# Performance work log

Measured on AMD Instinct MI355X. Metric: run time of the kernel, lower is better.

Reference implementation:

```python
import jax, jax.numpy as jnp
from jax import lax
import numpy as np
import math


def make_kernel():
    # StyleGAN2 blur kernel [1,3,3,1], normalized outer product
    k = jnp.array([1.0, 3.0, 3.0, 1.0], dtype=jnp.float32)
    k2 = jnp.outer(k, k)
    return k2 / jnp.sum(k2)


def upfirdn2d(x, kernel, up=1, pad=(0, 0)):
    # x: [B,C,H,W]; depthwise FIR filter, optional zero-insert upsampling
    C = x.shape[1]
    w = jnp.tile(jnp.flip(kernel)[None, None].astype(x.dtype), (C, 1, 1, 1))
    # torch upfirdn pads up-1 trailing zeros after the last sample; lhs_dilation
    # only inserts zeros between samples, so fold the extra zeros into pad[1].
    p = (pad[0], pad[1] + up - 1)
    return lax.conv_general_dilated(
        x, w, (1, 1), (p, p), lhs_dilation=(up, up), feature_group_count=C)


def modulated_conv(x, weight, style, demodulate=True, up=False):
    # per-sample weight modulation + demodulation, executed as grouped conv
    B, Cin, H, W = x.shape
    Cout, _, k, _ = weight.shape
    scale = 1.0 / math.sqrt(Cin * k * k)
    w = scale * weight[None] * style[:, None, :, None, None]  # [B,Cout,Cin,k,k]
    if demodulate:
        d = lax.rsqrt(jnp.sum(w * w, axis=(2, 3, 4)) + 1e-8)
        w = w * d[:, :, None, None, None]
    xg = x.reshape(1, B * Cin, H, W)
    if up:
        # conv_transpose2d(stride=2, pad=0) == lhs-dilated conv with flipped kernel
        wg = jnp.flip(w, (-2, -1)).reshape(B * Cout, Cin, k, k)
        out = lax.conv_general_dilated(
            xg, wg, (1, 1), ((k - 1, k - 1), (k - 1, k - 1)),
            lhs_dilation=(2, 2), feature_group_count=B)
    else:
        pad = k // 2
        out = lax.conv_general_dilated(
            xg, w.reshape(B * Cout, Cin, k, k), (1, 1),
            ((pad, pad), (pad, pad)), feature_group_count=B)
    return out.reshape(B, Cout, out.shape[2], out.shape[3])


def fused_lrelu(x, bias):
    y = x + bias[None, :, None, None]
    return jnp.where(y >= 0, y, 0.2 * y) * math.sqrt(2.0)


def setup_inputs() -> dict:
    key = jax.random.key(0)
    ks = jax.random.split(key, 12)
    B, C, H = 8, 512, 32
    f = jnp.float32
    return {
        "x": jax.random.normal(ks[0], (B, C, H, H), f),
        "skip": jax.random.normal(ks[1], (B, 3, H, H), f),
        "w1": jax.random.normal(ks[2], (C, C, 3, 3), f),
        "b1": jnp.zeros((C,), f),
        "s1": jax.random.normal(ks[3], (B, C), f),
        "nw1": jax.random.normal(ks[4], (1,), f) * 0.1,
        "n1": jax.random.normal(ks[5], (B, 1, 2 * H, 2 * H), f),
        "w2": jax.random.normal(ks[6], (C, C, 3, 3), f),
        "b2": jnp.zeros((C,), f),
        "s2": jax.random.normal(ks[7], (B, C), f),
        "nw2": jax.random.normal(ks[8], (1,), f) * 0.1,
        "n2": jax.random.normal(ks[9], (B, 1, 2 * H, 2 * H), f),
        "w_rgb": jax.random.normal(ks[10], (3, C, 1, 1), f),
        "b_rgb": jnp.zeros((3,), f),
        "s_rgb": jax.random.normal(ks[11], (B, C), f),
    }


def reference(x, skip, w1, b1, s1, nw1, n1, w2, b2, s2, nw2, n2,
              w_rgb, b_rgb, s_rgb):
    kern = make_kernel()
    # conv1: upsampling modulated conv + blur (Blur with upsample_factor=2)
    out = modulated_conv(x, w1, s1, demodulate=True, up=True)
    out = upfirdn2d(out, kern * 4.0, up=1, pad=(1, 1))
    out = out + nw1 * n1          # NoiseInjection
    out = fused_lrelu(out, b1)    # FusedLeakyReLU
    # conv2: plain modulated conv
    out = modulated_conv(out, w2, s2, demodulate=True)
    out = out + nw2 * n2
    out = fused_lrelu(out, b2)
    # ToRGB: 1x1 mod conv, no demodulation, + bias; skip = rgb + upsample(skip)
    rgb = modulated_conv(out, w_rgb, s_rgb, demodulate=False)
    rgb = rgb + b_rgb[None, :, None, None]
    skip_up = upfirdn2d(skip, kern * 4.0, up=2, pad=(2, 1))
    return rgb + skip_up
```

## Files before the change

### kernel.cpp

```cpp
#include <hip/hip_runtime.h>
#include <stdint.h>

typedef unsigned short ushort_t;
typedef unsigned int uint_t;
typedef __bf16 bf16x8 __attribute__((ext_vector_type(8)));
typedef float f32x4 __attribute__((ext_vector_type(4)));

#define GLOBAL_AS __attribute__((address_space(1)))
#define LDS_AS    __attribute__((address_space(3)))

#define SCALE_CONV 0.014731391f
#define SCALE_RGB  0.044194174f
#define SQRT2_F    1.41421356237f

__device__ __forceinline__ void async_cp16(const void* g, void* l) {
  __builtin_amdgcn_global_load_lds((const GLOBAL_AS uint_t*)g,
                                   (LDS_AS uint_t*)l, 16, 0, 0);
}
__device__ __forceinline__ ushort_t f2bf(float v) {
  union { float f; uint_t u; } c; c.f = v;
  uint_t r = c.u + 0x7fffu + ((c.u >> 16) & 1u);
  return (ushort_t)(r >> 16);
}
__device__ __forceinline__ float bf2f(ushort_t u) {
  union { uint_t u; float f; } c; c.u = ((uint_t)u) << 16;
  return c.f;
}

__global__ __launch_bounds__(256) void prep_x1(
    const float* __restrict__ x, const float* __restrict__ s1,
    ushort_t* __restrict__ xpad) {
  __shared__ ushort_t t[32 * 520];
  const int b  = blockIdx.x >> 5;
  const int j1 = blockIdx.x & 31;
  for (int idx = threadIdx.x; idx < 512 * 32; idx += 256) {
    int ci = idx >> 5, j2 = idx & 31;
    float v = x[(size_t)(b * 512 + ci) * 1024 + j1 * 32 + j2];
    v *= s1[b * 512 + ci] * SCALE_CONV;
    t[j2 * 520 + ci] = f2bf(v);
  }
  __syncthreads();
  for (int idx = threadIdx.x; idx < 32 * 512; idx += 256) {
    int j2 = idx >> 9, ci = idx & 511;
    xpad[((size_t)(b * 34 + j1 + 1) * 34 + (j2 + 1)) * 512 + ci] = t[j2 * 520 + ci];
  }
}

__global__ __launch_bounds__(256) void prep_w(
    const float* __restrict__ w1, const float* __restrict__ w2,
    ushort_t* __restrict__ wt1, ushort_t* __restrict__ wt2,
    float* __restrict__ wsqT1, float* __restrict__ wsqT2) {
  int t = blockIdx.x * 256 + threadIdx.x;
  const float* w  = (t < 262144) ? w1 : w2;
  ushort_t*   wt  = (t < 262144) ? wt1 : wt2;
  float*      wq  = (t < 262144) ? wsqT1 : wsqT2;
  int tt = t & 262143;
  int ci = tt & 511, co = tt >> 9;
  const float* wp = w + (size_t)(co * 512 + ci) * 9;
  float sq = 0.f;
#pragma unroll
  for (int u = 0; u < 9; ++u) {
    float v = wp[u];
    sq += v * v;
    wt[((size_t)u * 512 + co) * 512 + ci] = f2bf(v);
  }
  wq[ci * 512 + co] = sq;
}

__global__ __launch_bounds__(512) void demod2(
    const float* __restrict__ wsqT1, const float* __restrict__ s1, float* __restrict__ d1,
    const float* __restrict__ wsqT2, const float* __restrict__ s2, float* __restrict__ d2) {
  const float* wq = blockIdx.y ? wsqT2 : wsqT1;
  const float* s  = blockIdx.y ? s2 : s1;
  float*       d  = blockIdx.y ? d2 : d1;
  const int b  = blockIdx.x;
  const int co = threadIdx.x;
  __shared__ float ssq[512];
  float sv = s[b * 512 + co];
  ssq[co] = sv * sv;
  __syncthreads();
  float a = 0.f;
#pragma unroll 4
  for (int ci = 0; ci < 512; ++ci) a += wq[ci * 512 + co] * ssq[ci];
  d[b * 512 + co] = rsqrtf(a * (1.f / 4608.f) + 1e-8f);
}

__global__ __launch_bounds__(256) void border_zero(
    ushort_t* __restrict__ xpad, ushort_t* __restrict__ ypad, ushort_t* __restrict__ opad) {
  const int z = blockIdx.z;
  ushort_t* p = (z == 0) ? xpad : (z == 1 ? ypad : opad);
  const int W = (z == 0) ? 34 : (z == 1 ? 67 : 66);
  const int nb = 4 * W - 4;
  const int t = blockIdx.x * 256 + threadIdx.x;
  const int pix = t >> 6, ch = (t & 63) * 8;
  if (pix >= nb) return;
  const int b = blockIdx.y;
  int y, x;
  if (pix < W)          { y = 0;     x = pix; }
  else if (pix < 2 * W) { y = W - 1; x = pix - W; }
  else { int q = pix - 2 * W; y = 1 + (q >> 1); x = (q & 1) ? W - 1 : 0; }
  uint4 z4 = {0, 0, 0, 0};
  *(uint4*)(p + ((size_t)(b * W + y) * W + x) * 512 + ch) = z4;
}

__constant__ int           c_ph_off[4]  = {0, 4, 6, 8};
__constant__ int           c_ph_ntap[4] = {4, 2, 2, 1};
__constant__ unsigned char c_tap_u1[9]  = {0,0,1,1, 0,1, 1,1, 1};
__constant__ unsigned char c_tap_u2[9]  = {0,1,0,1, 1,1, 0,1, 1};
__constant__ unsigned char c_tap_pl[9]  = {8,6,2,0, 7,1, 5,3, 4};

template <int MODE>
__global__ __launch_bounds__(256, 3) void gemm_conv(
    const ushort_t* __restrict__ inp, const ushort_t* __restrict__ wt,
    const float* __restrict__ dmod, const float* __restrict__ noise,
    const float* __restrict__ nw, const float* __restrict__ bias,
    const float* __restrict__ snext, float snext_scale,
    ushort_t* __restrict__ outp) {
  __shared__ ushort_t ldsA[128 * 64];
  __shared__ ushort_t ldsB[128 * 64];

  const int tid  = threadIdx.x;
  const int lane = tid & 63;
  const int wv   = tid >> 6;
  const int wm   = wv & 1;
  const int wn   = wv >> 1;
  const int l16  = lane & 15;
  const int quad = lane >> 4;

  const int mtile = blockIdx.x;
  const int ntile = blockIdx.y;
  const int a  = (MODE == 0) ? blockIdx.z : 0;
  const int a1 = a >> 1, a2 = a & 1;

  const int cl = ((lane & 7) - (lane >> 3)) & 7;
  const char* pA[4];
  const char* pB[4];
#pragma unroll
  for (int t = 0; t < 4; ++t) {
    int row = wv * 32 + t * 8 + (lane >> 3);
    int m   = mtile * 128 + row;
    size_t pix;
    if (MODE == 0) {
      if (m > 8711) m = 8711;
      int b = m / 1089, rr = m % 1089;
      int p1 = rr / 33, p2 = rr % 33;
      pix = ((size_t)(b * 34 + p1) * 34 + p2) * 512;
    } else {
      int b = m >> 12, o1 = (m >> 6) & 63, o2 = m & 63;
      pix = ((size_t)(b * 66 + o1 + 1) * 66 + (o2 + 1)) * 512;
    }
    pA[t] = (const char*)inp + pix * 2 + cl * 16;
    int n = ntile * 128 + row;
    pB[t] = (const char*)wt + (size_t)n * 1024 + cl * 16;
  }
  char* dstA[4];
  char* dstB[4];
#pragma unroll
  for (int t = 0; t < 4; ++t) {
    dstA[t] = (char*)ldsA + wv * 4096 + t * 1024;
    dstB[t] = (char*)ldsB + wv * 4096 + t * 1024;
  }

  int offA[4], offB[4];
#pragma unroll
  for (int i = 0; i < 4; ++i) {
    int r  = wm * 64 + i * 16 + l16;
    int rn = wn * 64 + i * 16 + l16;
    offA[i] = r  * 64 + (((quad + r)  & 7) << 3);
    offB[i] = rn * 64 + (((quad + rn) & 7) << 3);
  }

  f32x4 acc[4][4];
#pragma unroll
  for (int i = 0; i < 4; ++i)
#pragma unroll
    for (int j = 0; j < 4; ++j) acc[i][j] = (f32x4){0.f, 0.f, 0.f, 0.f};

  const int ntap = (MODE == 0) ? c_ph_ntap[a] : 9;
#pragma unroll 1
  for (int ti = 0; ti < ntap; ++ti) {
    int aoff, boff;
    if (MODE == 0) {
      int e = c_ph_off[a] + ti;
      aoff = ((int)c_tap_u1[e] * 34 + (int)c_tap_u2[e]) * 1024;
      boff = (int)c_tap_pl[e] * 524288;
    } else {
      aoff = ((ti / 3 - 1) * 66 + (ti % 3 - 1)) * 1024;
      boff = ti * 524288;
    }
#pragma unroll 1
    for (int kc = 0; kc < 8; ++kc) {
      const int koff = kc * 128;
      __syncthreads();
#pragma unroll
      for (int t = 0; t < 4; ++t) async_cp16(pA[t] + aoff + koff, dstA[t]);
#pragma unroll
      for (int t = 0; t < 4; ++t) async_cp16(pB[t] + boff + koff, dstB[t]);
      __syncthreads();
#pragma unroll
      for (int kk = 0; kk < 2; ++kk) {
        const int kx = kk << 5;
        bf16x8 af[4], bg[4];
#pragma unroll
        for (int i = 0; i < 4; ++i) af[i] = *reinterpret_cast<const bf16x8*>(ldsA + (offA[i] ^ kx));
#pragma unroll
        for (int j = 0; j < 4; ++j) bg[j] = *reinterpret_cast<const bf16x8*>(ldsB + (offB[j] ^ kx));
#pragma unroll
        for (int i = 0; i < 4; ++i)
#pragma unroll
          for (int j = 0; j < 4; ++j)
            acc[i][j] = __builtin_amdgcn_mfma_f32_16x16x32_bf16(af[i], bg[j], acc[i][j], 0, 0, 0);
      }
    }
  }

  int co_[4];
#pragma unroll
  for (int j = 0; j < 4; ++j) co_[j] = ntile * 128 + wn * 64 + j * 16 + l16;

  if (MODE == 0) {
#pragma unroll
    for (int i = 0; i < 4; ++i) {
#pragma unroll
      for (int r = 0; r < 4; ++r) {
        int m = mtile * 128 + wm * 64 + i * 16 + quad * 4 + r;
        if (m < 8712) {
          int b = m / 1089, rr = m % 1089;
          int p1 = rr / 33, p2 = rr % 33;
          if ((a1 == 0 || p1 < 32) && (a2 == 0 || p2 < 32)) {
            int o1 = 2 * p1 + a1, o2 = 2 * p2 + a2;
            size_t ob = ((size_t)(b * 67 + o1 + 1) * 67 + (o2 + 1)) * 512;
#pragma unroll
            for (int j = 0; j < 4; ++j)
              outp[ob + co_[j]] = f2bf(acc[i][j][r] * dmod[b * 512 + co_[j]]);
          }
        }
      }
    }
  } else {
    const int b = mtile >> 5;
    const float nwv = nw[0];
    float dj_[4], sj_[4], bj_[4];
#pragma unroll
    for (int j = 0; j < 4; ++j) {
      dj_[j] = dmod[b * 512 + co_[j]];
      sj_[j] = snext[b * 512 + co_[j]] * snext_scale;
      bj_[j] = bias[co_[j]];
    }
#pragma unroll
    for (int i = 0; i < 4; ++i) {
#pragma unroll
      for (int r = 0; r < 4; ++r) {
        int m = mtile * 128 + wm * 64 + i * 16 + quad * 4 + r;
        int o1 = (m >> 6) & 63, o2 = m & 63;
        float nz = nwv * noise[(b << 12) + (o1 << 6) + o2];
        size_t ob = ((size_t)(b * 64 + o1) * 64 + o2) * 512;
#pragma unroll
        for (int j = 0; j < 4; ++j) {
          float v = acc[i][j][r] * dj_[j] + nz + bj_[j];
          v = (v >= 0.f ? v : 0.2f * v) * SQRT2_F;
          v *= sj_[j];
          outp[ob + co_[j]] = f2bf(v);
        }
      }
    }
  }
}

__global__ __launch_bounds__(256) void blur_noise_act(
    const ushort_t* __restrict__ y1pad, const float* __restrict__ noise,
    const float* __restrict__ nw, const float* __restrict__ bias,
    const float* __restrict__ s2, ushort_t* __restrict__ out1pad) {
  const int cg  = threadIdx.x & 63;
  const int pg  = blockIdx.x * 4 + (threadIdx.x >> 6);
  const int b   = pg >> 10;
  const int q1  = (pg >> 4) & 63;
  const int q2g = (pg & 15) * 4;
  const float cw[4] = {0.25f, 0.75f, 0.75f, 0.25f};

  float acc[4][8];
#pragma unroll
  for (int j = 0; j < 4; ++j)
#pragma unroll
    for (int e = 0; e < 8; ++e) acc[j][e] = 0.f;

#pragma unroll
  for (int t2 = 0; t2 < 7; ++t2) {
    int cc = q2g + t2;
    float vt[8];
#pragma unroll
    for (int e = 0; e < 8; ++e) vt[e] = 0.f;
#pragma unroll
    for (int t1 = 0; t1 < 4; ++t1) {
      const ushort_t* p = y1pad + ((size_t)(b * 67 + q1 + t1) * 67 + cc) * 512 + cg * 8;
      ushort_t v[8];
      *(uint4*)v = *(const uint4*)p;
#pragma unroll
      for (int e = 0; e < 8; ++e) vt[e] += cw[t1] * bf2f(v[e]);
    }
#pragma unroll
    for (int j = 0; j < 4; ++j) {
      int t = t2 - j;
      if (t >= 0 && t < 4) {
#pragma unroll
        for (int e = 0; e < 8; ++e) acc[j][e] += cw[t] * vt[e];
      }
    }
  }

  const float nwv = nw[0];
  float bj[8], sj[8];
#pragma unroll
  for (int e = 0; e < 8; ++e) {
    bj[e] = bias[cg * 8 + e];
    sj[e] = s2[b * 512 + cg * 8 + e] * SCALE_CONV;
  }
#pragma unroll
  for (int j = 0; j < 4; ++j) {
    int q2 = q2g + j;
    float nz = nwv * noise[(b << 12) + (q1 << 6) + q2];
    ushort_t o[8];
#pragma unroll
    for (int e = 0; e < 8; ++e) {
      float v = acc[j][e] + nz + bj[e];
      v = (v >= 0.f ? v : 0.2f * v) * SQRT2_F * sj[e];
      o[e] = f2bf(v);
    }
    *(uint4*)(out1pad + ((size_t)(b * 66 + q1 + 1) * 66 + (q2 + 1)) * 512 + cg * 8) = *(uint4*)o;
  }
}

__global__ __launch_bounds__(256) void torgb_skip(
    const ushort_t* __restrict__ out2s, const float* __restrict__ wrgb,
    const float* __restrict__ brgb, const float* __restrict__ skip,
    float* __restrict__ out) {
  const int lane = threadIdx.x & 63;
  const int pix  = blockIdx.x * 4 + (threadIdx.x >> 6);
  const int b = pix >> 12, o1 = (pix >> 6) & 63, o2 = pix & 63;
  const ushort_t* src = out2s + (size_t)pix * 512 + lane * 8;
  ushort_t v[8];
  *(uint4*)v = *(const uint4*)src;
  float s0 = 0.f, s1 = 0.f, s2 = 0.f;
#pragma unroll
  for (int e = 0; e < 8; ++e) {
    float xv = bf2f(v[e]);
    int ci = lane * 8 + e;
    s0 += xv * wrgb[ci];
    s1 += xv * wrgb[512 + ci];
    s2 += xv * wrgb[1024 + ci];
  }
#pragma unroll
  for (int o = 32; o; o >>= 1) {
    s0 += __shfl_xor(s0, o);
    s1 += __shfl_xor(s1, o);
    s2 += __shfl_xor(s2, o);
  }
  if (lane < 3) {
    float v3 = (lane == 0) ? s0 : (lane == 1 ? s1 : s2);
    int P1 = o1 >> 1, P2 = o2 >> 1;
    int jy0, jy1, jx0, jx1;
    float wy0, wy1, wx0, wx1;
    if ((o1 & 1) == 0) { jy0 = P1 - 1; wy0 = .25f; jy1 = P1;     wy1 = .75f; }
    else               { jy0 = P1;     wy0 = .75f; jy1 = P1 + 1; wy1 = .25f; }
    if ((o2 & 1) == 0) { jx0 = P2 - 1; wx0 = .25f; jx1 = P2;     wx1 = .75f; }
    else               { jx0 = P2;     wx0 = .75f; jx1 = P2 + 1; wx1 = .25f; }
    const float* sp = skip + (size_t)(b * 3 + lane) * 1024;
    float sv = 0.f;
    if (jy0 >= 0 && jy0 < 32) {
      if (jx0 >= 0 && jx0 < 32) sv += wy0 * wx0 * sp[jy0 * 32 + jx0];
      if (jx1 >= 0 && jx1 < 32) sv += wy0 * wx1 * sp[jy0 * 32 + jx1];
    }
    if (jy1 >= 0 && jy1 < 32) {
      if (jx0 >= 0 && jx0 < 32) sv += wy1 * wx0 * sp[jy1 * 32 + jx0];
      if (jx1 >= 0 && jx1 < 32) sv += wy1 * wx1 * sp[jy1 * 32 + jx1];
    }
    out[((size_t)(b * 3 + lane) << 12) + (o1 << 6) + o2] = v3 + brgb[lane] + sv;
  }
}

extern "C" void kernel_launch(void* const* d_in, const int* in_sizes, int n_in,
                              void* d_out, int out_size, void* d_ws, size_t ws_size,
                              hipStream_t stream) {
  const float* x    = (const float*)d_in[0];
  const float* skip = (const float*)d_in[1];
  const float* w1   = (const float*)d_in[2];
  const float* b1   = (const float*)d_in[3];
  const float* s1   = (const float*)d_in[4];
  const float* nw1  = (const float*)d_in[5];
  const float* n1   = (const float*)d_in[6];
  const float* w2   = (const float*)d_in[7];
  const float* b2   = (const float*)d_in[8];
  const float* s2   = (const float*)d_in[9];
  const float* nw2  = (const float*)d_in[10];
  const float* n2   = (const float*)d_in[11];
  const float* wrgb = (const float*)d_in[12];
  const float* brgb = (const float*)d_in[13];
  const float* srgb = (const float*)d_in[14];

  char* ws = (char*)d_ws;
  const size_t XPAD_B  = (size_t)8 * 34 * 34 * 512 * 2;
  const size_t Y1PAD_B = (size_t)8 * 67 * 67 * 512 * 2;
  const size_t OUT1_B  = (size_t)8 * 66 * 66 * 512 * 2;
  const size_t WT_B    = (size_t)9 * 512 * 512 * 2;
  size_t off = 0;
  ushort_t* xpad1   = (ushort_t*)(ws + off); off += XPAD_B;
  ushort_t* y1pad   = (ushort_t*)(ws + off); off += Y1PAD_B;
  ushort_t* out1pad = (ushort_t*)(ws + off); off += OUT1_B;
  ushort_t* wt1     = (ushort_t*)(ws + off); off += WT_B;
  ushort_t* wt2     = (ushort_t*)(ws + off); off += WT_B;
  float*    d1      = (float*)(ws + off);    off += 8 * 512 * 4;
  float*    d2      = (float*)(ws + off);    off += 8 * 512 * 4;
  ushort_t* out2s  = y1pad;
  float*    wsqT1  = (float*)y1pad;
  float*    wsqT2  = wsqT1 + 512 * 512;

  prep_x1<<<256, 256, 0, stream>>>(x, s1, xpad1);
  prep_w<<<2048, 256, 0, stream>>>(w1, w2, wt1, wt2, wsqT1, wsqT2);
  demod2<<<dim3(8, 2), 512, 0, stream>>>(wsqT1, s1, d1, wsqT2, s2, d2);
  border_zero<<<dim3(66, 8, 3), 256, 0, stream>>>(xpad1, y1pad, out1pad);

  gemm_conv<0><<<dim3(69, 4, 4), 256, 0, stream>>>(
      xpad1, wt1, d1, nullptr, nullptr, nullptr, nullptr, 0.f, y1pad);
  blur_noise_act<<<2048, 256, 0, stream>>>(y1pad, n1, nw1, b1, s2, out1pad);
  gemm_conv<1><<<dim3(256, 4, 1), 256, 0, stream>>>(
      out1pad, wt2, d2, n2, nw2, b2, srgb, SCALE_RGB, out2s);
  torgb_skip<<<8192, 256, 0, stream>>>(out2s, wrgb, brgb, skip, (float*)d_out);
}
```

Before: 393.8 us.

## Double-buffer LDS in conv2 GEMM to overlap async loads with MFMA

Splits the templated GEMM into two kernels and gives the second 3x3 conv a double-buffered LDS pipeline over a flattened 72-step tap×K loop. The next stage's global-to-LDS async copies are issued before computing on the current buffer, with partial vmcnt waits, so load latency can overlap the MFMA work. LDS use doubles and occupancy is lowered to 2 blocks per CU. Hand-written s_barrier and waitcnt asm adds risk if the compiler reorders or counts loads differently.

```diff
diff --git a/kernel.cpp b/kernel.cpp
--- a/kernel.cpp
+++ b/kernel.cpp
@@ -109,13 +109,9 @@
 __constant__ unsigned char c_tap_u2[9]  = {0,1,0,1, 1,1, 0,1, 1};
 __constant__ unsigned char c_tap_pl[9]  = {8,6,2,0, 7,1, 5,3, 4};
 
-template <int MODE>
-__global__ __launch_bounds__(256, 3) void gemm_conv(
+__global__ __launch_bounds__(256, 3) void gemm_conv1(
     const ushort_t* __restrict__ inp, const ushort_t* __restrict__ wt,
-    const float* __restrict__ dmod, const float* __restrict__ noise,
-    const float* __restrict__ nw, const float* __restrict__ bias,
-    const float* __restrict__ snext, float snext_scale,
-    ushort_t* __restrict__ outp) {
+    const float* __restrict__ dmod, ushort_t* __restrict__ outp) {
   __shared__ ushort_t ldsA[128 * 64];
   __shared__ ushort_t ldsB[128 * 64];
 
@@ -129,7 +125,7 @@
 
   const int mtile = blockIdx.x;
   const int ntile = blockIdx.y;
-  const int a  = (MODE == 0) ? blockIdx.z : 0;
+  const int a  = blockIdx.z;
   const int a1 = a >> 1, a2 = a & 1;
 
   const int cl = ((lane & 7) - (lane >> 3)) & 7;
@@ -139,16 +135,10 @@
   for (int t = 0; t < 4; ++t) {
     int row = wv * 32 + t * 8 + (lane >> 3);
     int m   = mtile * 128 + row;
-    size_t pix;
-    if (MODE == 0) {
-      if (m > 8711) m = 8711;
-      int b = m / 1089, rr = m % 1089;
-      int p1 = rr / 33, p2 = rr % 33;
-      pix = ((size_t)(b * 34 + p1) * 34 + p2) * 512;
-    } else {
-      int b = m >> 12, o1 = (m >> 6) & 63, o2 = m & 63;
-      pix = ((size_t)(b * 66 + o1 + 1) * 66 + (o2 + 1)) * 512;
-    }
+    if (m > 8711) m = 8711;
+    int b = m / 1089, rr = m % 1089;
+    int p1 = rr / 33, p2 = rr % 33;
+    size_t pix = ((size_t)(b * 34 + p1) * 34 + p2) * 512;
     pA[t] = (const char*)inp + pix * 2 + cl * 16;
     int n = ntile * 128 + row;
     pB[t] = (const char*)wt + (size_t)n * 1024 + cl * 16;
@@ -176,18 +166,12 @@
 #pragma unroll
     for (int j = 0; j < 4; ++j) acc[i][j] = (f32x4){0.f, 0.f, 0.f, 0.f};
 
-  const int ntap = (MODE == 0) ? c_ph_ntap[a] : 9;
+  const int ntap = c_ph_ntap[a];
 #pragma unroll 1
   for (int ti = 0; ti < ntap; ++ti) {
-    int aoff, boff;
-    if (MODE == 0) {
-      int e = c_ph_off[a] + ti;
-      aoff = ((int)c_tap_u1[e] * 34 + (int)c_tap_u2[e]) * 1024;
-      boff = (int)c_tap_pl[e] * 524288;
-    } else {
-      aoff = ((ti / 3 - 1) * 66 + (ti % 3 - 1)) * 1024;
-      boff = ti * 524288;
-    }
+    int e = c_ph_off[a] + ti;
+    int aoff = ((int)c_tap_u1[e] * 34 + (int)c_tap_u2[e]) * 1024;
+    int boff = (int)c_tap_pl[e] * 524288;
 #pragma unroll 1
     for (int kc = 0; kc < 8; ++kc) {
       const int koff = kc * 128;
@@ -218,50 +202,144 @@
 #pragma unroll
   for (int j = 0; j < 4; ++j) co_[j] = ntile * 128 + wn * 64 + j * 16 + l16;
 
-  if (MODE == 0) {
-#pragma unroll
-    for (int i = 0; i < 4; ++i) {
-#pragma unroll
-      for (int r = 0; r < 4; ++r) {
-        int m = mtile * 128 + wm * 64 + i * 16 + quad * 4 + r;
-        if (m < 8712) {
-          int b = m / 1089, rr = m % 1089;
-          int p1 = rr / 33, p2 = rr % 33;
-          if ((a1 == 0 || p1 < 32) && (a2 == 0 || p2 < 32)) {
-            int o1 = 2 * p1 + a1, o2 = 2 * p2 + a2;
-            size_t ob = ((size_t)(b * 67 + o1 + 1) * 67 + (o2 + 1)) * 512;
-#pragma unroll
-            for (int j = 0; j < 4; ++j)
-              outp[ob + co_[j]] = f2bf(acc[i][j][r] * dmod[b * 512 + co_[j]]);
-          }
+#pragma unroll
+  for (int i = 0; i < 4; ++i) {
+#pragma unroll
+    for (int r = 0; r < 4; ++r) {
+      int m = mtile * 128 + wm * 64 + i * 16 + quad * 4 + r;
+      if (m < 8712) {
+        int b = m / 1089, rr = m % 1089;
+        int p1 = rr / 33, p2 = rr % 33;
+        if ((a1 == 0 || p1 < 32) && (a2 == 0 || p2 < 32)) {
+          int o1 = 2 * p1 + a1, o2 = 2 * p2 + a2;
+          size_t ob = ((size_t)(b * 67 + o1 + 1) * 67 + (o2 + 1)) * 512;
+#pragma unroll
+          for (int j = 0; j < 4; ++j)
+            outp[ob + co_[j]] = f2bf(acc[i][j][r] * dmod[b * 512 + co_[j]]);
         }
       }
     }
-  } else {
-    const int b = mtile >> 5;
-    const float nwv = nw[0];
-    float dj_[4], sj_[4], bj_[4];
-#pragma unroll
-    for (int j = 0; j < 4; ++j) {
-      dj_[j] = dmod[b * 512 + co_[j]];
-      sj_[j] = snext[b * 512 + co_[j]] * snext_scale;
-      bj_[j] = bias[co_[j]];
-    }
-#pragma unroll
-    for (int i = 0; i < 4; ++i) {
-#pragma unroll
-      for (int r = 0; r < 4; ++r) {
-        int m = mtile * 128 + wm * 64 + i * 16 + quad * 4 + r;
-        int o1 = (m >> 6) & 63, o2 = m & 63;
-        float nz = nwv * noise[(b << 12) + (o1 << 6) + o2];
-        size_t ob = ((size_t)(b * 64 + o1) * 64 + o2) * 512;
-#pragma unroll
-        for (int j = 0; j < 4; ++j) {
-          float v = acc[i][j][r] * dj_[j] + nz + bj_[j];
-          v = (v >= 0.f ? v : 0.2f * v) * SQRT2_F;
-          v *= sj_[j];
-          outp[ob + co_[j]] = f2bf(v);
-        }
+  }
+}
+
+__global__ __launch_bounds__(256, 2) void gemm_conv2_pipe(
+    const ushort_t* __restrict__ inp, const ushort_t* __restrict__ wt,
+    const float* __restrict__ dmod, const float* __restrict__ noise,
+    const float* __restrict__ nw, const float* __restrict__ bias,
+    const float* __restrict__ snext, float snext_scale,
+    ushort_t* __restrict__ outp) {
+  __shared__ ushort_t ldsA[2 * 128 * 64];
+  __shared__ ushort_t ldsB[2 * 128 * 64];
+
+  const int tid  = threadIdx.x;
+  const int lane = tid & 63;
+  const int wv   = tid >> 6;
+  const int wm   = wv & 1;
+  const int wn   = wv >> 1;
+  const int l16  = lane & 15;
+  const int quad = lane >> 4;
+
+  const int mtile = blockIdx.x;
+  const int ntile = blockIdx.y;
+
+  const int cl = ((lane & 7) - (lane >> 3)) & 7;
+  const char* pA[4];
+  const char* pB[4];
+#pragma unroll
+  for (int t = 0; t < 4; ++t) {
+    int row = wv * 32 + t * 8 + (lane >> 3);
+    int m   = mtile * 128 + row;
+    int b = m >> 12, o1 = (m >> 6) & 63, o2 = m & 63;
+    size_t pix = ((size_t)(b * 66 + o1 + 1) * 66 + (o2 + 1)) * 512;
+    pA[t] = (const char*)inp + pix * 2 + cl * 16;
+    int n = ntile * 128 + row;
+    pB[t] = (const char*)wt + (size_t)n * 1024 + cl * 16;
+  }
+
+  int offA[4], offB[4];
+#pragma unroll
+  for (int i = 0; i < 4; ++i) {
+    int r  = wm * 64 + i * 16 + l16;
+    int rn = wn * 64 + i * 16 + l16;
+    offA[i] = r  * 64 + (((quad + r)  & 7) << 3);
+    offB[i] = rn * 64 + (((quad + rn) & 7) << 3);
+  }
+
+  f32x4 acc[4][4];
+#pragma unroll
+  for (int i = 0; i < 4; ++i)
+#pragma unroll
+    for (int j = 0; j < 4; ++j) acc[i][j] = (f32x4){0.f, 0.f, 0.f, 0.f};
+
+  auto stagef = [&](int k, int sel) {
+    int tap = k >> 3, kc = k & 7;
+    int ty = tap * 86 >> 8;
+    int tx = tap - ty * 3;
+    int aoff = ((ty - 1) * 66 + (tx - 1)) * 1024 + kc * 128;
+    int boff = tap * 524288 + kc * 128;
+    char* dA = (char*)ldsA + sel * 16384 + wv * 4096;
+    char* dB = (char*)ldsB + sel * 16384 + wv * 4096;
+#pragma unroll
+    for (int t = 0; t < 4; ++t) async_cp16(pA[t] + aoff, dA + t * 1024);
+#pragma unroll
+    for (int t = 0; t < 4; ++t) async_cp16(pB[t] + boff, dB + t * 1024);
+  };
+
+  stagef(0, 0);
+#pragma unroll 1
+  for (int k = 0; k < 72; ++k) {
+    asm volatile("s_barrier" ::: "memory");
+    if (k < 71) {
+      stagef(k + 1, (k + 1) & 1);
+      asm volatile("s_waitcnt vmcnt(8)" ::: "memory");
+    } else {
+      asm volatile("s_waitcnt vmcnt(0)" ::: "memory");
+    }
+    asm volatile("s_barrier" ::: "memory");
+    const ushort_t* bA = ldsA + (k & 1) * 8192;
+    const ushort_t* bB = ldsB + (k & 1) * 8192;
+#pragma unroll
+    for (int kk = 0; kk < 2; ++kk) {
+      const int kx = kk << 5;
+      bf16x8 af[4], bg[4];
+#pragma unroll
+      for (int i = 0; i < 4; ++i) af[i] = *reinterpret_cast<const bf16x8*>(bA + (offA[i] ^ kx));
+#pragma unroll
+      for (int j = 0; j < 4; ++j) bg[j] = *reinterpret_cast<const bf16x8*>(bB + (offB[j] ^ kx));
+#pragma unroll
+      for (int i = 0; i < 4; ++i)
+#pragma unroll
+        for (int j = 0; j < 4; ++j)
+          acc[i][j] = __builtin_amdgcn_mfma_f32_16x16x32_bf16(af[i], bg[j], acc[i][j], 0, 0, 0);
+    }
+  }
+
+  const int b = mtile >> 5;
+  int co_[4];
+#pragma unroll
+  for (int j = 0; j < 4; ++j) co_[j] = ntile * 128 + wn * 64 + j * 16 + l16;
+  const float nwv = nw[0];
+  float dj_[4], sj_[4], bj_[4];
+#pragma unroll
+  for (int j = 0; j < 4; ++j) {
+    dj_[j] = dmod[b * 512 + co_[j]];
+    sj_[j] = snext[b * 512 + co_[j]] * snext_scale;
+    bj_[j] = bias[co_[j]];
+  }
+#pragma unroll
+  for (int i = 0; i < 4; ++i) {
+#pragma unroll
+    for (int r = 0; r < 4; ++r) {
+      int m = mtile * 128 + wm * 64 + i * 16 + quad * 4 + r;
+      int o1 = (m >> 6) & 63, o2 = m & 63;
+      float nz = nwv * noise[(b << 12) + (o1 << 6) + o2];
+      size_t ob = ((size_t)(b * 64 + o1) * 64 + o2) * 512;
+#pragma unroll
+      for (int j = 0; j < 4; ++j) {
+        float v = acc[i][j][r] * dj_[j] + nz + bj_[j];
+        v = (v >= 0.f ? v : 0.2f * v) * SQRT2_F;
+        v *= sj_[j];
+        outp[ob + co_[j]] = f2bf(v);
       }
     }
   }
@@ -419,10 +497,9 @@
   demod2<<<dim3(8, 2), 512, 0, stream>>>(wsqT1, s1, d1, wsqT2, s2, d2);
   border_zero<<<dim3(66, 8, 3), 256, 0, stream>>>(xpad1, y1pad, out1pad);
 
-  gemm_conv<0><<<dim3(69, 4, 4), 256, 0, stream>>>(
-      xpad1, wt1, d1, nullptr, nullptr, nullptr, nullptr, 0.f, y1pad);
+  gemm_conv1<<<dim3(69, 4, 4), 256, 0, stream>>>(xpad1, wt1, d1, y1pad);
   blur_noise_act<<<2048, 256, 0, stream>>>(y1pad, n1, nw1, b1, s2, out1pad);
-  gemm_conv<1><<<dim3(256, 4, 1), 256, 0, stream>>>(
+  gemm_conv2_pipe<<<dim3(256, 4), 256, 0, stream>>>(
       out1pad, wt2, d2, n2, nw2, b2, srgb, SCALE_RGB, out2s);
   torgb_skip<<<8192, 256, 0, stream>>>(out2s, wrgb, brgb, skip, (float*)d_out);
 }
```

Measured after the change: 407.0 us. 3.4% more time.

## Double-buffer GEMM K loop, fuse ToRGB into conv2 epilogue, split demod

Applied to the files above, without the earlier changes.

Restructures the implicit-GEMM conv kernel to use a 32-wide K step with double-buffered LDS. The next chunk is prefetched asynchronously while the current one feeds the MFMAs, and occupancy is raised to 4 blocks. The conv2 epilogue now does the 1x1 ToRGB projection directly, reducing across lanes and atomically adding into a small fp32 buffer. This removes the bf16 write and re-read of the full 512-channel activation. A light finish kernel adds bias and the upsampled skip, and the demod kernel is split across more blocks; float atomics make the summation order nondeterministic.

```diff
diff --git a/kernel.cpp b/kernel.cpp
--- a/kernel.cpp
+++ b/kernel.cpp
@@ -67,27 +67,47 @@
   wq[ci * 512 + co] = sq;
 }
 
-__global__ __launch_bounds__(512) void demod2(
+__global__ __launch_bounds__(256) void demod3(
     const float* __restrict__ wsqT1, const float* __restrict__ s1, float* __restrict__ d1,
     const float* __restrict__ wsqT2, const float* __restrict__ s2, float* __restrict__ d2) {
-  const float* wq = blockIdx.y ? wsqT2 : wsqT1;
-  const float* s  = blockIdx.y ? s2 : s1;
-  float*       d  = blockIdx.y ? d2 : d1;
-  const int b  = blockIdx.x;
-  const int co = threadIdx.x;
+  const float* wq = blockIdx.z ? wsqT2 : wsqT1;
+  const float* s  = blockIdx.z ? s2 : s1;
+  float*       d  = blockIdx.z ? d2 : d1;
+  const int b   = blockIdx.y;
+  const int co  = blockIdx.x * 64 + (threadIdx.x & 63);
+  const int cig = threadIdx.x >> 6;
   __shared__ float ssq[512];
-  float sv = s[b * 512 + co];
-  ssq[co] = sv * sv;
+  __shared__ float red[4][64];
+  for (int i = threadIdx.x; i < 512; i += 256) {
+    float v = s[b * 512 + i];
+    ssq[i] = v * v;
+  }
   __syncthreads();
   float a = 0.f;
 #pragma unroll 4
-  for (int ci = 0; ci < 512; ++ci) a += wq[ci * 512 + co] * ssq[ci];
-  d[b * 512 + co] = rsqrtf(a * (1.f / 4608.f) + 1e-8f);
+  for (int ci = cig * 128; ci < cig * 128 + 128; ++ci)
+    a += wq[ci * 512 + co] * ssq[ci];
+  red[cig][threadIdx.x & 63] = a;
+  __syncthreads();
+  if (cig == 0) {
+    int l = threadIdx.x & 63;
+    float tot = red[0][l] + red[1][l] + red[2][l] + red[3][l];
+    d[b * 512 + co] = rsqrtf(tot * (1.f / 4608.f) + 1e-8f);
+  }
 }
 
 __global__ __launch_bounds__(256) void border_zero(
-    ushort_t* __restrict__ xpad, ushort_t* __restrict__ ypad, ushort_t* __restrict__ opad) {
+    ushort_t* __restrict__ xpad, ushort_t* __restrict__ ypad, ushort_t* __restrict__ opad,
+    float* __restrict__ rgbpart) {
   const int z = blockIdx.z;
+  if (z == 3) {
+    int i = (blockIdx.y * 66 + blockIdx.x) * 256 + threadIdx.x;
+    if (i < 24576) {
+      uint4 z4 = {0, 0, 0, 0};
+      *(uint4*)(rgbpart + i * 4) = z4;
+    }
+    return;
+  }
   ushort_t* p = (z == 0) ? xpad : (z == 1 ? ypad : opad);
   const int W = (z == 0) ? 34 : (z == 1 ? 67 : 66);
   const int nb = 4 * W - 4;
@@ -110,14 +130,14 @@
 __constant__ unsigned char c_tap_pl[9]  = {8,6,2,0, 7,1, 5,3, 4};
 
 template <int MODE>
-__global__ __launch_bounds__(256, 3) void gemm_conv(
+__global__ __launch_bounds__(256, 4) void gemm_conv_p(
     const ushort_t* __restrict__ inp, const ushort_t* __restrict__ wt,
     const float* __restrict__ dmod, const float* __restrict__ noise,
     const float* __restrict__ nw, const float* __restrict__ bias,
-    const float* __restrict__ snext, float snext_scale,
-    ushort_t* __restrict__ outp) {
-  __shared__ ushort_t ldsA[128 * 64];
-  __shared__ ushort_t ldsB[128 * 64];
+    const float* __restrict__ srgb, const float* __restrict__ wrgb,
+    float* __restrict__ rgbpart, ushort_t* __restrict__ outp) {
+  __shared__ ushort_t ldsA[2 * 4096];
+  __shared__ ushort_t ldsB[2 * 4096];
 
   const int tid  = threadIdx.x;
   const int lane = tid & 63;
@@ -131,13 +151,15 @@
   const int ntile = blockIdx.y;
   const int a  = (MODE == 0) ? blockIdx.z : 0;
   const int a1 = a >> 1, a2 = a & 1;
-
-  const int cl = ((lane & 7) - (lane >> 3)) & 7;
-  const char* pA[4];
-  const char* pB[4];
-#pragma unroll
-  for (int t = 0; t < 4; ++t) {
-    int row = wv * 32 + t * 8 + (lane >> 3);
+  const int phoff = (MODE == 0) ? c_ph_off[a] : 0;
+  const int nk    = (MODE == 0) ? c_ph_ntap[a] * 16 : 144;
+
+  const int cl = ((lane & 3) - (lane >> 3)) & 3;
+  const char* pA[2];
+  const char* pB[2];
+#pragma unroll
+  for (int t = 0; t < 2; ++t) {
+    int row = wv * 32 + t * 16 + (lane >> 2);
     int m   = mtile * 128 + row;
     size_t pix;
     if (MODE == 0) {
@@ -153,21 +175,14 @@
     int n = ntile * 128 + row;
     pB[t] = (const char*)wt + (size_t)n * 1024 + cl * 16;
   }
-  char* dstA[4];
-  char* dstB[4];
-#pragma unroll
-  for (int t = 0; t < 4; ++t) {
-    dstA[t] = (char*)ldsA + wv * 4096 + t * 1024;
-    dstB[t] = (char*)ldsB + wv * 4096 + t * 1024;
-  }
 
   int offA[4], offB[4];
 #pragma unroll
   for (int i = 0; i < 4; ++i) {
     int r  = wm * 64 + i * 16 + l16;
     int rn = wn * 64 + i * 16 + l16;
-    offA[i] = r  * 64 + (((quad + r)  & 7) << 3);
-    offB[i] = rn * 64 + (((quad + rn) & 7) << 3);
+    offA[i] = r  * 32 + (((quad + (r  >> 1)) & 3) << 3);
+    offB[i] = rn * 32 + (((quad + (rn >> 1)) & 3) << 3);
   }
 
   f32x4 acc[4][4];
@@ -176,42 +191,50 @@
 #pragma unroll
     for (int j = 0; j < 4; ++j) acc[i][j] = (f32x4){0.f, 0.f, 0.f, 0.f};
 
-  const int ntap = (MODE == 0) ? c_ph_ntap[a] : 9;
-#pragma unroll 1
-  for (int ti = 0; ti < ntap; ++ti) {
+  auto stagef = [&](int kn, int sel) {
+    int tap = kn >> 4, kc = kn & 15;
     int aoff, boff;
     if (MODE == 0) {
-      int e = c_ph_off[a] + ti;
-      aoff = ((int)c_tap_u1[e] * 34 + (int)c_tap_u2[e]) * 1024;
-      boff = (int)c_tap_pl[e] * 524288;
+      int e = phoff + tap;
+      aoff = ((int)c_tap_u1[e] * 34 + (int)c_tap_u2[e]) * 1024 + kc * 64;
+      boff = (int)c_tap_pl[e] * 524288 + kc * 64;
     } else {
-      aoff = ((ti / 3 - 1) * 66 + (ti % 3 - 1)) * 1024;
-      boff = ti * 524288;
-    }
+      int ty = (tap * 86) >> 8;
+      int tx = tap - ty * 3;
+      aoff = ((ty - 1) * 66 + (tx - 1)) * 1024 + kc * 64;
+      boff = tap * 524288 + kc * 64;
+    }
+    char* dA = (char*)ldsA + sel * 8192 + wv * 2048;
+    char* dB = (char*)ldsB + sel * 8192 + wv * 2048;
+#pragma unroll
+    for (int t = 0; t < 2; ++t) async_cp16(pA[t] + aoff, dA + t * 1024);
+#pragma unroll
+    for (int t = 0; t < 2; ++t) async_cp16(pB[t] + boff, dB + t * 1024);
+  };
+
+  stagef(0, 0);
 #pragma unroll 1
-    for (int kc = 0; kc < 8; ++kc) {
-      const int koff = kc * 128;
-      __syncthreads();
-#pragma unroll
-      for (int t = 0; t < 4; ++t) async_cp16(pA[t] + aoff + koff, dstA[t]);
-#pragma unroll
-      for (int t = 0; t < 4; ++t) async_cp16(pB[t] + boff + koff, dstB[t]);
-      __syncthreads();
-#pragma unroll
-      for (int kk = 0; kk < 2; ++kk) {
-        const int kx = kk << 5;
-        bf16x8 af[4], bg[4];
-#pragma unroll
-        for (int i = 0; i < 4; ++i) af[i] = *reinterpret_cast<const bf16x8*>(ldsA + (offA[i] ^ kx));
-#pragma unroll
-        for (int j = 0; j < 4; ++j) bg[j] = *reinterpret_cast<const bf16x8*>(ldsB + (offB[j] ^ kx));
-#pragma unroll
-        for (int i = 0; i < 4; ++i)
-#pragma unroll
-          for (int j = 0; j < 4; ++j)
-            acc[i][j] = __builtin_amdgcn_mfma_f32_16x16x32_bf16(af[i], bg[j], acc[i][j], 0, 0, 0);
-      }
-    }
+  for (int k = 0; k < nk; ++k) {
+    asm volatile("s_barrier" ::: "memory");
+    if (k + 1 < nk) {
+      stagef(k + 1, (k + 1) & 1);
+      asm volatile("s_waitcnt vmcnt(4)" ::: "memory");
+    } else {
+      asm volatile("s_waitcnt vmcnt(0)" ::: "memory");
+    }
+    asm volatile("s_barrier" ::: "memory");
+    const ushort_t* bA = ldsA + (k & 1) * 4096;
+    const ushort_t* bB = ldsB + (k & 1) * 4096;
+    bf16x8 af[4], bg[4];
+#pragma unroll
+    for (int i = 0; i < 4; ++i) af[i] = *reinterpret_cast<const bf16x8*>(bA + offA[i]);
+#pragma unroll
+    for (int j = 0; j < 4; ++j) bg[j] = *reinterpret_cast<const bf16x8*>(bB + offB[j]);
+#pragma unroll
+    for (int i = 0; i < 4; ++i)
+#pragma unroll
+      for (int j = 0; j < 4; ++j)
+        acc[i][j] = __builtin_amdgcn_mfma_f32_16x16x32_bf16(af[i], bg[j], acc[i][j], 0, 0, 0);
   }
 
   int co_[4];
@@ -240,12 +263,14 @@
   } else {
     const int b = mtile >> 5;
     const float nwv = nw[0];
-    float dj_[4], sj_[4], bj_[4];
+    float dj_[4], sj_[4], bj_[4], wr[3][4];
 #pragma unroll
     for (int j = 0; j < 4; ++j) {
       dj_[j] = dmod[b * 512 + co_[j]];
-      sj_[j] = snext[b * 512 + co_[j]] * snext_scale;
+      sj_[j] = srgb[b * 512 + co_[j]] * SCALE_RGB;
       bj_[j] = bias[co_[j]];
+#pragma unroll
+      for (int c = 0; c < 3; ++c) wr[c][j] = wrgb[c * 512 + co_[j]];
     }
 #pragma unroll
     for (int i = 0; i < 4; ++i) {
@@ -254,13 +279,21 @@
         int m = mtile * 128 + wm * 64 + i * 16 + quad * 4 + r;
         int o1 = (m >> 6) & 63, o2 = m & 63;
         float nz = nwv * noise[(b << 12) + (o1 << 6) + o2];
-        size_t ob = ((size_t)(b * 64 + o1) * 64 + o2) * 512;
+        float vv[4];
 #pragma unroll
         for (int j = 0; j < 4; ++j) {
           float v = acc[i][j][r] * dj_[j] + nz + bj_[j];
           v = (v >= 0.f ? v : 0.2f * v) * SQRT2_F;
-          v *= sj_[j];
-          outp[ob + co_[j]] = f2bf(v);
+          vv[j] = v * sj_[j];
+        }
+#pragma unroll
+        for (int c = 0; c < 3; ++c) {
+          float s = vv[0] * wr[c][0] + vv[1] * wr[c][1] + vv[2] * wr[c][2] + vv[3] * wr[c][3];
+          s += __shfl_xor(s, 1);
+          s += __shfl_xor(s, 2);
+          s += __shfl_xor(s, 4);
+          s += __shfl_xor(s, 8);
+          if (l16 == 0) atomicAdd(&rgbpart[c * 32768 + m], s);
         }
       }
     }
@@ -330,52 +363,31 @@
   }
 }
 
-__global__ __launch_bounds__(256) void torgb_skip(
-    const ushort_t* __restrict__ out2s, const float* __restrict__ wrgb,
-    const float* __restrict__ brgb, const float* __restrict__ skip,
-    float* __restrict__ out) {
-  const int lane = threadIdx.x & 63;
-  const int pix  = blockIdx.x * 4 + (threadIdx.x >> 6);
-  const int b = pix >> 12, o1 = (pix >> 6) & 63, o2 = pix & 63;
-  const ushort_t* src = out2s + (size_t)pix * 512 + lane * 8;
-  ushort_t v[8];
-  *(uint4*)v = *(const uint4*)src;
-  float s0 = 0.f, s1 = 0.f, s2 = 0.f;
-#pragma unroll
-  for (int e = 0; e < 8; ++e) {
-    float xv = bf2f(v[e]);
-    int ci = lane * 8 + e;
-    s0 += xv * wrgb[ci];
-    s1 += xv * wrgb[512 + ci];
-    s2 += xv * wrgb[1024 + ci];
-  }
-#pragma unroll
-  for (int o = 32; o; o >>= 1) {
-    s0 += __shfl_xor(s0, o);
-    s1 += __shfl_xor(s1, o);
-    s2 += __shfl_xor(s2, o);
-  }
-  if (lane < 3) {
-    float v3 = (lane == 0) ? s0 : (lane == 1 ? s1 : s2);
-    int P1 = o1 >> 1, P2 = o2 >> 1;
-    int jy0, jy1, jx0, jx1;
-    float wy0, wy1, wx0, wx1;
-    if ((o1 & 1) == 0) { jy0 = P1 - 1; wy0 = .25f; jy1 = P1;     wy1 = .75f; }
-    else               { jy0 = P1;     wy0 = .75f; jy1 = P1 + 1; wy1 = .25f; }
-    if ((o2 & 1) == 0) { jx0 = P2 - 1; wx0 = .25f; jx1 = P2;     wx1 = .75f; }
-    else               { jx0 = P2;     wx0 = .75f; jx1 = P2 + 1; wx1 = .25f; }
-    const float* sp = skip + (size_t)(b * 3 + lane) * 1024;
-    float sv = 0.f;
-    if (jy0 >= 0 && jy0 < 32) {
-      if (jx0 >= 0 && jx0 < 32) sv += wy0 * wx0 * sp[jy0 * 32 + jx0];
-      if (jx1 >= 0 && jx1 < 32) sv += wy0 * wx1 * sp[jy0 * 32 + jx1];
-    }
-    if (jy1 >= 0 && jy1 < 32) {
-      if (jx0 >= 0 && jx0 < 32) sv += wy1 * wx0 * sp[jy1 * 32 + jx0];
-      if (jx1 >= 0 && jx1 < 32) sv += wy1 * wx1 * sp[jy1 * 32 + jx1];
-    }
-    out[((size_t)(b * 3 + lane) << 12) + (o1 << 6) + o2] = v3 + brgb[lane] + sv;
-  }
+__global__ __launch_bounds__(256) void rgb_finish(
+    const float* __restrict__ rgbpart, const float* __restrict__ brgb,
+    const float* __restrict__ skip, float* __restrict__ out) {
+  const int t = blockIdx.x * 256 + threadIdx.x;
+  if (t >= 98304) return;
+  const int m = t & 32767, c = t >> 15;
+  const int b = m >> 12, o1 = (m >> 6) & 63, o2 = m & 63;
+  int P1 = o1 >> 1, P2 = o2 >> 1;
+  int jy0, jy1, jx0, jx1;
+  float wy0, wy1, wx0, wx1;
+  if ((o1 & 1) == 0) { jy0 = P1 - 1; wy0 = .25f; jy1 = P1;     wy1 = .75f; }
+  else               { jy0 = P1;     wy0 = .75f; jy1 = P1 + 1; wy1 = .25f; }
+  if ((o2 & 1) == 0) { jx0 = P2 - 1; wx0 = .25f; jx1 = P2;     wx1 = .75f; }
+  else               { jx0 = P2;     wx0 = .75f; jx1 = P2 + 1; wx1 = .25f; }
+  const float* sp = skip + (size_t)(b * 3 + c) * 1024;
+  float sv = 0.f;
+  if (jy0 >= 0 && jy0 < 32) {
+    if (jx0 >= 0 && jx0 < 32) sv += wy0 * wx0 * sp[jy0 * 32 + jx0];
+    if (jx1 >= 0 && jx1 < 32) sv += wy0 * wx1 * sp[jy0 * 32 + jx1];
+  }
+  if (jy1 >= 0 && jy1 < 32) {
+    if (jx0 >= 0 && jx0 < 32) sv += wy1 * wx0 * sp[jy1 * 32 + jx0];
+    if (jx1 >= 0 && jx1 < 32) sv += wy1 * wx1 * sp[jy1 * 32 + jx1];
+  }
+  out[((size_t)(b * 3 + c) << 12) + (o1 << 6) + o2] = rgbpart[c * 32768 + m] + brgb[c] + sv;
 }
 
 extern "C" void kernel_launch(void* const* d_in, const int* in_sizes, int n_in,
@@ -410,19 +422,19 @@
   ushort_t* wt2     = (ushort_t*)(ws + off); off += WT_B;
   float*    d1      = (float*)(ws + off);    off += 8 * 512 * 4;
   float*    d2      = (float*)(ws + off);    off += 8 * 512 * 4;
-  ushort_t* out2s  = y1pad;
+  float*    rgbpart = (float*)(ws + off);    off += 3 * 32768 * 4;
   float*    wsqT1  = (float*)y1pad;
   float*    wsqT2  = wsqT1 + 512 * 512;
 
   prep_x1<<<256, 256, 0, stream>>>(x, s1, xpad1);
   prep_w<<<2048, 256, 0, stream>>>(w1, w2, wt1, wt2, wsqT1, wsqT2);
-  demod2<<<dim3(8, 2), 512, 0, stream>>>(wsqT1, s1, d1, wsqT2, s2, d2);
-  border_zero<<<dim3(66, 8, 3), 256, 0, stream>>>(xpad1, y1pad, out1pad);
-
-  gemm_conv<0><<<dim3(69, 4, 4), 256, 0, stream>>>(
-      xpad1, wt1, d1, nullptr, nullptr, nullptr, nullptr, 0.f, y1pad);
+  demod3<<<dim3(8, 8, 2), 256, 0, stream>>>(wsqT1, s1, d1, wsqT2, s2, d2);
+  border_zero<<<dim3(66, 8, 4), 256, 0, stream>>>(xpad1, y1pad, out1pad, rgbpart);
+
+  gemm_conv_p<0><<<dim3(69, 4, 4), 256, 0, stream>>>(
+      xpad1, wt1, d1, nullptr, nullptr, nullptr, nullptr, nullptr, nullptr, y1pad);
   blur_noise_act<<<2048, 256, 0, stream>>>(y1pad, n1, nw1, b1, s2, out1pad);
-  gemm_conv<1><<<dim3(256, 4, 1), 256, 0, stream>>>(
-      out1pad, wt2, d2, n2, nw2, b2, srgb, SCALE_RGB, out2s);
-  torgb_skip<<<8192, 256, 0, stream>>>(out2s, wrgb, brgb, skip, (float*)d_out);
-}
+  gemm_conv_p<1><<<dim3(256, 4), 256, 0, stream>>>(
+      out1pad, wt2, d2, n2, nw2, b2, srgb, wrgb, rgbpart, nullptr);
+  rgb_finish<<<384, 256, 0, stream>>>(rgbpart, brgb, skip, (float*)d_out);
+}
```

Result: slower. 408.4 us (+3.7%).
